# Kernel tuning notes

Hardware: AMD Instinct MI355X
Metric: run time of the kernel (lower is better)

Reference implementation:

```python
import jax, jax.numpy as jnp
import numpy as np

N_HEAD = 8


def setup_inputs() -> dict:
    key = jax.random.key(0)
    ks = jax.random.split(key, 4)
    B, L, C = 4, 1024, 512
    x = jax.random.normal(ks[0], (B, L, C), dtype=jnp.float32)
    adj = jax.random.uniform(ks[1], (B, L, L), dtype=jnp.float32)
    W_qkv = jax.random.normal(ks[2], (3 * C, C), dtype=jnp.float32) * 0.02
    W_proj = jax.random.normal(ks[3], (C, C), dtype=jnp.float32) * 0.02
    bias_scale = jnp.array([3.0, 3.0], dtype=jnp.float32)
    beta = jnp.ones((3,), dtype=jnp.float32) / 3.0
    return {"x": x, "adj": adj, "W_qkv": W_qkv, "W_proj": W_proj,
            "bias_scale": bias_scale, "beta": beta}


def _branch_attn(Q, K, V, scale, bias=None):
    # Q,K,V: [B,H,L,D]
    S = jnp.einsum('bhqd,bhkd->bhqk', Q, K) / scale
    if bias is not None:
        S = S + bias
    attn = jax.nn.softmax(S, axis=-1)
    return jnp.einsum('bhqk,bhkd->bhqd', attn, V)


def reference(x, adj, W_qkv, W_proj, bias_scale, beta):
    B, L, C = x.shape
    H = N_HEAD
    D = C // H
    scale = jnp.sqrt(jnp.float32(D))

    qkv = x @ W_qkv.T  # [B,L,3C]
    Q, K, V = jnp.split(qkv, 3, axis=-1)
    Q = Q.reshape(B, L, H, D).transpose(0, 2, 1, 3)  # [B,H,L,D]
    K = K.reshape(B, L, H, D).transpose(0, 2, 1, 3)
    V = V.reshape(B, L, H, D).transpose(0, 2, 1, 3)

    # has_cls: zero out CLS row/col in adjacency
    adj_local = adj.at[:, 0, :].set(0.0).at[:, :, 0].set(0.0)
    B_fwd = adj_local[:, None, :, :]              # [B,1,L,L]
    B_bwd = jnp.swapaxes(adj_local, -1, -2)[:, None, :, :]

    h0 = _branch_attn(Q, K, V, scale)
    h1 = _branch_attn(Q, K, V, scale, bias_scale[0] * B_fwd)
    h2 = _branch_attn(Q, K, V, scale, bias_scale[1] * B_bwd)

    b = jax.nn.softmax(beta, axis=0)
    out = b[0] * h0 + b[1] * h1 + b[2] * h2      # [B,H,L,D]
    out = out.transpose(0, 2, 1, 3).reshape(B, L, C)
    return out @ W_proj.T
```

## Files before the change

### kernel.cpp

```cpp
#include <hip/hip_runtime.h>
#include <hip/hip_bf16.h>
#include <stdint.h>

#define B_  4
#define L_  1024
#define C_  512
#define H_  8
#define D_  64
#define BH_ 32
#define M_  4096

typedef short  bf16x8 __attribute__((ext_vector_type(8)));
typedef float  f32x4  __attribute__((ext_vector_type(4)));
typedef unsigned short u16x8 __attribute__((ext_vector_type(8)));
typedef unsigned int   u32x2 __attribute__((ext_vector_type(2)));

__device__ __forceinline__ unsigned short f2bf(float f) {
    union { float f; uint32_t u; } v; v.f = f;
    uint32_t u = v.u;
    return (unsigned short)((u + 0x7fffu + ((u >> 16) & 1u)) >> 16);
}
__device__ __forceinline__ float bf2f(unsigned short s) {
    union { uint32_t u; float f; } v; v.u = ((uint32_t)s) << 16;
    return v.f;
}

__device__ __forceinline__ void gload16(const void* g, void* s) {
    __builtin_amdgcn_global_load_lds((const __attribute__((address_space(1))) void*)g,
                                     (__attribute__((address_space(3))) void*)s, 16, 0, 0);
}

__global__ void cvt_bf16(const float* __restrict__ in, unsigned short* __restrict__ out, int n4) {
    int i = blockIdx.x * blockDim.x + threadIdx.x;
    if (i < n4) {
        float4 v = ((const float4*)in)[i];
        ushort4 o;
        o.x = f2bf(v.x); o.y = f2bf(v.y); o.z = f2bf(v.z); o.w = f2bf(v.w);
        ((ushort4*)out)[i] = o;
    }
}

__global__ __launch_bounds__(256) void prep_e(const float* __restrict__ adj,
                                              const float* __restrict__ bias_scale,
                                              unsigned short* __restrict__ EI) {
    __shared__ float Tr[64][65];
    const int b = blockIdx.z, q0 = blockIdx.y * 64, k0 = blockIdx.x * 64;
    const float* adjb = adj + (size_t)b * L_ * L_;
    const int tid = threadIdx.x;
#pragma unroll
    for (int i = 0; i < 4; ++i) {
        int idx = i * 256 + tid;
        int rk = idx >> 4, c4 = (idx & 15) * 4;
        float4 v = *(const float4*)(adjb + (size_t)(k0 + rk) * L_ + q0 + c4);
        Tr[rk][c4 + 0] = v.x; Tr[rk][c4 + 1] = v.y; Tr[rk][c4 + 2] = v.z; Tr[rk][c4 + 3] = v.w;
    }
    __syncthreads();
    const float bs0 = bias_scale[0], bs1 = bias_scale[1];
    const int w = tid >> 6, l = tid & 63, g = l >> 4, c = l & 15;
#pragma unroll
    for (int qs = 0; qs < 4; ++qs) {
        int ql = qs * 16 + c, qg = q0 + ql;
        int klb = w * 16 + g * 4;
        float4 af4 = *(const float4*)(adjb + (size_t)qg * L_ + k0 + klb);
        unsigned short ef[4], eb[4];
        const float afv[4] = {af4.x, af4.y, af4.z, af4.w};
#pragma unroll
        for (int i = 0; i < 4; ++i) {
            int kg = k0 + klb + i;
            bool z = (qg == 0) || (kg == 0);
            ef[i] = f2bf(z ? 1.0f : __expf(bs0 * afv[i]));
            eb[i] = f2bf(z ? 1.0f : __expf(bs1 * Tr[klb + i][ql]));
        }
        size_t o = (((size_t)b * 64 + (blockIdx.y * 4 + qs)) * 64 + (blockIdx.x * 4 + w)) * 512 + (size_t)l * 8;
        u16x8 o8 = {ef[0], ef[1], ef[2], ef[3], eb[0], eb[1], eb[2], eb[3]};
        *(u16x8*)(EI + o) = o8;
    }
}

template <int KDIM, int NDIM, int EPI>
__global__ __launch_bounds__(256, 2) void gemm_bf16(const unsigned short* __restrict__ Amat,
                                                    const unsigned short* __restrict__ Bmat,
                                                    float* __restrict__ outp,
                                                    unsigned short* __restrict__ q_out,
                                                    unsigned short* __restrict__ k_out,
                                                    unsigned short* __restrict__ v_out) {
    __shared__ __align__(16) unsigned short As[128 * 64];
    __shared__ __align__(16) unsigned short Bs[128 * 64];
    const int tid = threadIdx.x;
    const int l = tid & 63, wid = tid >> 6;
    const int g = l >> 4, c = l & 15;
    const int wr = wid >> 1, wc = wid & 1;
    const int row0 = blockIdx.y * 128, col0 = blockIdx.x * 128;

    f32x4 acc[4][4];
#pragma unroll
    for (int mi = 0; mi < 4; ++mi)
#pragma unroll
        for (int ni = 0; ni < 4; ++ni) acc[mi][ni] = (f32x4){0.f, 0.f, 0.f, 0.f};

    for (int k0 = 0; k0 < KDIM; k0 += 64) {
        bf16x8 ra[4], rb[4];
#pragma unroll
        for (int i = 0; i < 4; ++i) {
            int q = i * 256 + tid;
            int r = q >> 3, cb = (q & 7) * 16;
            ra[i] = *(const bf16x8*)((const char*)Amat + (size_t)(row0 + r) * (KDIM * 2) + k0 * 2 + cb);
            rb[i] = *(const bf16x8*)((const char*)Bmat + (size_t)(col0 + r) * (KDIM * 2) + k0 * 2 + cb);
        }
        __syncthreads();
#pragma unroll
        for (int i = 0; i < 4; ++i) {
            int q = i * 256 + tid;
            int r = q >> 3, cb = (q & 7) * 16;
            int sw = cb ^ ((r & 7) << 4);
            *(bf16x8*)((char*)As + r * 128 + sw) = ra[i];
            *(bf16x8*)((char*)Bs + r * 128 + sw) = rb[i];
        }
        __syncthreads();
#pragma unroll
        for (int kk = 0; kk < 2; ++kk) {
            bf16x8 afr[4], bfr[4];
#pragma unroll
            for (int mi = 0; mi < 4; ++mi) {
                int r = wr * 64 + mi * 16 + c;
                afr[mi] = *(const bf16x8*)((const char*)As + r * 128 + ((kk * 64 + g * 16) ^ ((r & 7) << 4)));
            }
#pragma unroll
            for (int ni = 0; ni < 4; ++ni) {
                int r = wc * 64 + ni * 16 + c;
                bfr[ni] = *(const bf16x8*)((const char*)Bs + r * 128 + ((kk * 64 + g * 16) ^ ((r & 7) << 4)));
            }
#pragma unroll
            for (int mi = 0; mi < 4; ++mi)
#pragma unroll
                for (int ni = 0; ni < 4; ++ni)
                    acc[mi][ni] = __builtin_amdgcn_mfma_f32_16x16x32_bf16(afr[mi], bfr[ni], acc[mi][ni], 0, 0, 0);
        }
    }
#pragma unroll
    for (int mi = 0; mi < 4; ++mi) {
#pragma unroll
        for (int ni = 0; ni < 4; ++ni) {
#pragma unroll
            for (int ii = 0; ii < 4; ++ii) {
                int m = row0 + wr * 64 + mi * 16 + g * 4 + ii;
                int n = col0 + wc * 64 + ni * 16 + c;
                float val = acc[mi][ni][ii];
                if (EPI == 0) {
                    unsigned short v = f2bf(val);
                    int b = m >> 10, ll = m & 1023;
                    int which = n >> 9, cc = n & 511;
                    int hh = cc >> 6, d = cc & 63;
                    int bh = b * 8 + hh;
                    if (which == 0)      q_out[((size_t)bh * L_ + ll) * D_ + d] = v;
                    else if (which == 1) k_out[((size_t)bh * L_ + ll) * D_ + d] = v;
                    else                 v_out[((size_t)bh * D_ + d) * L_ + ll] = v;
                } else {
                    outp[(size_t)m * NDIM + n] = val;
                }
            }
        }
    }
}

__global__ __launch_bounds__(256, 2) void attn_kernel(const unsigned short* __restrict__ Qb,
                                                      const unsigned short* __restrict__ Kb,
                                                      const unsigned short* __restrict__ Vtb,
                                                      const unsigned short* __restrict__ EI,
                                                      const float* __restrict__ beta,
                                                      unsigned short* __restrict__ hb) {
    __shared__ __align__(16) char smem[2][32768];
    const int tid = threadIdx.x;
    const int w = tid >> 6, l = tid & 63;
    const int g = l >> 4, c = l & 15;
    const int bh = blockIdx.y, b = bh >> 3;
    const int q0 = blockIdx.x * 64 + w * 16;
    const int qt = blockIdx.x * 4 + w;

    const unsigned short* Qrow = Qb + ((size_t)bh * L_ + q0 + c) * D_;
    const bf16x8 qf0 = *(const bf16x8*)(Qrow + g * 8);
    const bf16x8 qf1 = *(const bf16x8*)(Qrow + 32 + g * 8);

    const unsigned short* Kbase = Kb + (size_t)bh * L_ * D_;
    const unsigned short* Vbase = Vtb + (size_t)bh * D_ * L_;
    const unsigned short* Ebase = EI + ((size_t)(b * 64 + qt) * 64) * 512;

    f32x4 O[3][4];
#pragma unroll
    for (int j = 0; j < 3; ++j)
#pragma unroll
        for (int dc = 0; dc < 4; ++dc) O[j][dc] = (f32x4){0.f, 0.f, 0.f, 0.f};
    float lsum0 = 0.f, lsum1 = 0.f, lsum2 = 0.f;

    const int srow = l >> 3, sm = l & 7;
    const int key = (c & 7) << 4;

    auto stage = [&](int t, char* base) {
#pragma unroll
        for (int n = 0; n < 2; ++n) {
            int i = 2 * w + n;
            int row = i * 8 + srow;
            int sw = (sm ^ (row & 7)) * 8;
            gload16(Kbase + (size_t)(t * 64 + row) * D_ + sw, base + i * 1024);
            gload16(Vbase + (size_t)row * L_ + t * 64 + sw, base + 8192 + i * 1024);
        }
#pragma unroll
        for (int ks = 0; ks < 4; ++ks)
            gload16(Ebase + (size_t)(t * 4 + ks) * 512 + l * 8, base + 16384 + w * 4096 + ks * 1024);
    };

    auto compute = [&](char* base) {
        char* Kl = base;
        char* Vl = base + 8192;
        char* El = base + 16384 + w * 4096;
        bf16x8 efr[4];
#pragma unroll
        for (int ks = 0; ks < 4; ++ks) efr[ks] = *(const bf16x8*)(El + ks * 1024 + l * 16);

        unsigned r[4][3][2];
#pragma unroll
        for (int st = 0; st < 4; ++st) {
            const char* kr = Kl + (st * 16 + c) * 128;
            bf16x8 ka = *(const bf16x8*)(kr + ((g * 16) ^ key));
            bf16x8 kb = *(const bf16x8*)(kr + ((64 + g * 16) ^ key));
            f32x4 s = (f32x4){0.f, 0.f, 0.f, 0.f};
            s = __builtin_amdgcn_mfma_f32_16x16x32_bf16(ka, qf0, s, 0, 0, 0);
            s = __builtin_amdgcn_mfma_f32_16x16x32_bf16(kb, qf1, s, 0, 0, 0);
            float p[3][4];
#pragma unroll
            for (int i = 0; i < 4; ++i) {
                float p0 = __expf(s[i] * 0.125f);
                float p1 = p0 * bf2f((unsigned short)efr[st][i]);
                float p2 = p0 * bf2f((unsigned short)efr[st][4 + i]);
                lsum0 += p0; lsum1 += p1; lsum2 += p2;
                p[0][i] = p0; p[1][i] = p1; p[2][i] = p2;
            }
#pragma unroll
            for (int j = 0; j < 3; ++j) {
                r[st][j][0] = __builtin_amdgcn_perm(__float_as_uint(p[j][1]), __float_as_uint(p[j][0]), 0x07060302u);
                r[st][j][1] = __builtin_amdgcn_perm(__float_as_uint(p[j][3]), __float_as_uint(p[j][2]), 0x07060302u);
            }
        }
#pragma unroll
        for (int kk = 0; kk < 2; ++kk) {
            bf16x8 af[3];
#pragma unroll
            for (int j = 0; j < 3; ++j) {
                union { unsigned u[4]; bf16x8 v; } t_;
                t_.u[0] = r[2 * kk][j][0];     t_.u[1] = r[2 * kk][j][1];
                t_.u[2] = r[2 * kk + 1][j][0]; t_.u[3] = r[2 * kk + 1][j][1];
                af[j] = t_.v;
            }
#pragma unroll
            for (int dc = 0; dc < 4; ++dc) {
                const char* vr = Vl + (dc * 16 + c) * 128;
                u32x2 vlo = *(const u32x2*)(vr + ((kk * 64 + g * 8) ^ key));
                u32x2 vhi = *(const u32x2*)(vr + ((kk * 64 + 32 + g * 8) ^ key));
                union { unsigned u[4]; bf16x8 v; } bv;
                bv.u[0] = vlo[0]; bv.u[1] = vlo[1]; bv.u[2] = vhi[0]; bv.u[3] = vhi[1];
#pragma unroll
                for (int j = 0; j < 3; ++j)
                    O[j][dc] = __builtin_amdgcn_mfma_f32_16x16x32_bf16(af[j], bv.v, O[j][dc], 0, 0, 0);
            }
        }
    };

    stage(0, smem[0]);
    __syncthreads();
#pragma unroll 1
    for (int t = 0; t < 16; t += 2) {
        stage(t + 1, smem[1]);
        compute(smem[0]);
        __syncthreads();
        if (t + 2 < 16) stage(t + 2, smem[0]);
        compute(smem[1]);
        __syncthreads();
    }

    lsum0 += __shfl_xor(lsum0, 16); lsum0 += __shfl_xor(lsum0, 32);
    lsum1 += __shfl_xor(lsum1, 16); lsum1 += __shfl_xor(lsum1, 32);
    lsum2 += __shfl_xor(lsum2, 16); lsum2 += __shfl_xor(lsum2, 32);

    float b0 = beta[0], b1 = beta[1], b2 = beta[2];
    float bm = fmaxf(b0, fmaxf(b1, b2));
    float e0 = __expf(b0 - bm), e1 = __expf(b1 - bm), e2 = __expf(b2 - bm);
    float inv = 1.0f / (e0 + e1 + e2);
    float i0 = e0 * inv / lsum0, i1 = e1 * inv / lsum1, i2 = e2 * inv / lsum2;

    float iq0[4], iq1[4], iq2[4];
#pragma unroll
    for (int ii = 0; ii < 4; ++ii) {
        iq0[ii] = __shfl(i0, g * 4 + ii);
        iq1[ii] = __shfl(i1, g * 4 + ii);
        iq2[ii] = __shfl(i2, g * 4 + ii);
    }
    const int hcol = (bh & 7) * 64;
#pragma unroll
    for (int dc = 0; dc < 4; ++dc) {
#pragma unroll
        for (int ii = 0; ii < 4; ++ii) {
            float h = iq0[ii] * O[0][dc][ii] + iq1[ii] * O[1][dc][ii] + iq2[ii] * O[2][dc][ii];
            int qrow = q0 + g * 4 + ii;
            hb[((size_t)(b << 10) + qrow) * C_ + hcol + dc * 16 + c] = f2bf(h);
        }
    }
}

extern "C" void kernel_launch(void* const* d_in, const int* in_sizes, int n_in,
                              void* d_out, int out_size, void* d_ws, size_t ws_size,
                              hipStream_t stream) {
    const float* x          = (const float*)d_in[0];
    const float* adj        = (const float*)d_in[1];
    const float* wqkv       = (const float*)d_in[2];
    const float* wproj      = (const float*)d_in[3];
    const float* bias_scale = (const float*)d_in[4];
    const float* beta       = (const float*)d_in[5];
    float* out = (float*)d_out;

    char* ws = (char*)d_ws;
    size_t off = 0;
    auto alloc = [&](size_t bytes) {
        void* p = ws + off;
        off += (bytes + 255) & ~(size_t)255;
        return p;
    };
    unsigned short* xb     = (unsigned short*)alloc((size_t)M_ * C_ * 2);
    unsigned short* wqkvb  = (unsigned short*)alloc((size_t)3 * C_ * C_ * 2);
    unsigned short* wprojb = (unsigned short*)alloc((size_t)C_ * C_ * 2);
    unsigned short* Qb     = (unsigned short*)alloc((size_t)BH_ * L_ * D_ * 2);
    unsigned short* Kb     = (unsigned short*)alloc((size_t)BH_ * L_ * D_ * 2);
    unsigned short* Vtb    = (unsigned short*)alloc((size_t)BH_ * D_ * L_ * 2);
    unsigned short* EI     = (unsigned short*)alloc((size_t)B_ * L_ * L_ * 4);
    unsigned short* hb     = (unsigned short*)alloc((size_t)M_ * C_ * 2);

    {
        int n4 = M_ * C_ / 4;
        cvt_bf16<<<(n4 + 255) / 256, 256, 0, stream>>>(x, xb, n4);
    }
    {
        int n4 = 3 * C_ * C_ / 4;
        cvt_bf16<<<(n4 + 255) / 256, 256, 0, stream>>>(wqkv, wqkvb, n4);
    }
    {
        int n4 = C_ * C_ / 4;
        cvt_bf16<<<(n4 + 255) / 256, 256, 0, stream>>>(wproj, wprojb, n4);
    }
    prep_e<<<dim3(L_ / 64, L_ / 64, B_), 256, 0, stream>>>(adj, bias_scale, EI);
    gemm_bf16<512, 1536, 0><<<dim3(1536 / 128, M_ / 128), 256, 0, stream>>>(xb, wqkvb, nullptr, Qb, Kb, Vtb);
    attn_kernel<<<dim3(L_ / 64, BH_), 256, 0, stream>>>(Qb, Kb, Vtb, EI, beta, hb);
    gemm_bf16<512, 512, 1><<<dim3(512 / 128, M_ / 128), 256, 0, stream>>>(hb, wprojb, out, nullptr, nullptr, nullptr);
}
```

Before: 82.15 us.

## Fuse conversions, shrink GEMM tiles, remap attention grid, load bias via registers

```diff
diff --git a/kernel.cpp b/kernel.cpp
--- a/kernel.cpp
+++ b/kernel.cpp
@@ -30,14 +30,23 @@
                                      (__attribute__((address_space(3))) void*)s, 16, 0, 0);
 }
 
-__global__ void cvt_bf16(const float* __restrict__ in, unsigned short* __restrict__ out, int n4) {
-    int i = blockIdx.x * blockDim.x + threadIdx.x;
-    if (i < n4) {
-        float4 v = ((const float4*)in)[i];
-        ushort4 o;
-        o.x = f2bf(v.x); o.y = f2bf(v.y); o.z = f2bf(v.z); o.w = f2bf(v.w);
-        ((ushort4*)out)[i] = o;
-    }
+#define NX4   (M_ * C_ / 4)
+#define NWQ4  (3 * C_ * C_ / 4)
+#define NWP4  (C_ * C_ / 4)
+__global__ void cvt_all(const float* __restrict__ x, const float* __restrict__ wq,
+                        const float* __restrict__ wp,
+                        unsigned short* __restrict__ xb, unsigned short* __restrict__ wqb,
+                        unsigned short* __restrict__ wpb) {
+    int i = blockIdx.x * 256 + threadIdx.x;
+    const float* src; unsigned short* dst; int o;
+    if (i < NX4) { src = x; dst = xb; o = i; }
+    else if (i < NX4 + NWQ4) { src = wq; dst = wqb; o = i - NX4; }
+    else if (i < NX4 + NWQ4 + NWP4) { src = wp; dst = wpb; o = i - NX4 - NWQ4; }
+    else return;
+    float4 v = ((const float4*)src)[o];
+    ushort4 r;
+    r.x = f2bf(v.x); r.y = f2bf(v.y); r.z = f2bf(v.z); r.w = f2bf(v.w);
+    ((ushort4*)dst)[o] = r;
 }
 
 __global__ __launch_bounds__(256) void prep_e(const float* __restrict__ adj,
@@ -77,74 +86,85 @@
     }
 }
 
-template <int KDIM, int NDIM, int EPI>
-__global__ __launch_bounds__(256, 2) void gemm_bf16(const unsigned short* __restrict__ Amat,
+template <int BM, int BN, int KDIM, int EPI, int NDIM>
+__global__ __launch_bounds__(256, 4) void gemm_bf16(const unsigned short* __restrict__ Amat,
                                                     const unsigned short* __restrict__ Bmat,
                                                     float* __restrict__ outp,
                                                     unsigned short* __restrict__ q_out,
                                                     unsigned short* __restrict__ k_out,
                                                     unsigned short* __restrict__ v_out) {
-    __shared__ __align__(16) unsigned short As[128 * 64];
-    __shared__ __align__(16) unsigned short Bs[128 * 64];
+    constexpr int NA = BM / 32, NB = BN / 32;
+    constexpr int MI = BM / 32, NI = BN / 32;
+    __shared__ __align__(16) unsigned short As[BM * 64];
+    __shared__ __align__(16) unsigned short Bs[BN * 64];
     const int tid = threadIdx.x;
     const int l = tid & 63, wid = tid >> 6;
     const int g = l >> 4, c = l & 15;
     const int wr = wid >> 1, wc = wid & 1;
-    const int row0 = blockIdx.y * 128, col0 = blockIdx.x * 128;
-
-    f32x4 acc[4][4];
-#pragma unroll
-    for (int mi = 0; mi < 4; ++mi)
-#pragma unroll
-        for (int ni = 0; ni < 4; ++ni) acc[mi][ni] = (f32x4){0.f, 0.f, 0.f, 0.f};
+    const int row0 = blockIdx.y * BM, col0 = blockIdx.x * BN;
+
+    f32x4 acc[MI][NI];
+#pragma unroll
+    for (int mi = 0; mi < MI; ++mi)
+#pragma unroll
+        for (int ni = 0; ni < NI; ++ni) acc[mi][ni] = (f32x4){0.f, 0.f, 0.f, 0.f};
 
     for (int k0 = 0; k0 < KDIM; k0 += 64) {
-        bf16x8 ra[4], rb[4];
-#pragma unroll
-        for (int i = 0; i < 4; ++i) {
+        bf16x8 ra[NA], rb[NB];
+#pragma unroll
+        for (int i = 0; i < NA; ++i) {
             int q = i * 256 + tid;
             int r = q >> 3, cb = (q & 7) * 16;
             ra[i] = *(const bf16x8*)((const char*)Amat + (size_t)(row0 + r) * (KDIM * 2) + k0 * 2 + cb);
-            rb[i] = *(const bf16x8*)((const char*)Bmat + (size_t)(col0 + r) * (KDIM * 2) + k0 * 2 + cb);
-        }
-        __syncthreads();
-#pragma unroll
-        for (int i = 0; i < 4; ++i) {
+        }
+#pragma unroll
+        for (int i = 0; i < NB; ++i) {
             int q = i * 256 + tid;
             int r = q >> 3, cb = (q & 7) * 16;
-            int sw = cb ^ ((r & 7) << 4);
-            *(bf16x8*)((char*)As + r * 128 + sw) = ra[i];
-            *(bf16x8*)((char*)Bs + r * 128 + sw) = rb[i];
+            rb[i] = *(const bf16x8*)((const char*)Bmat + (size_t)(col0 + r) * (KDIM * 2) + k0 * 2 + cb);
         }
         __syncthreads();
 #pragma unroll
+        for (int i = 0; i < NA; ++i) {
+            int q = i * 256 + tid;
+            int r = q >> 3, cb = (q & 7) * 16;
+            *(bf16x8*)((char*)As + r * 128 + (cb ^ ((r & 7) << 4))) = ra[i];
+        }
+#pragma unroll
+        for (int i = 0; i < NB; ++i) {
+            int q = i * 256 + tid;
+            int r = q >> 3, cb = (q & 7) * 16;
+            *(bf16x8*)((char*)Bs + r * 128 + (cb ^ ((r & 7) << 4))) = rb[i];
+        }
+        __syncthreads();
+#pragma unroll
         for (int kk = 0; kk < 2; ++kk) {
-            bf16x8 afr[4], bfr[4];
-#pragma unroll
-            for (int mi = 0; mi < 4; ++mi) {
-                int r = wr * 64 + mi * 16 + c;
+            bf16x8 afr[MI], bfr[NI];
+#pragma unroll
+            for (int mi = 0; mi < MI; ++mi) {
+                int r = wr * (BM / 2) + mi * 16 + c;
                 afr[mi] = *(const bf16x8*)((const char*)As + r * 128 + ((kk * 64 + g * 16) ^ ((r & 7) << 4)));
             }
 #pragma unroll
-            for (int ni = 0; ni < 4; ++ni) {
-                int r = wc * 64 + ni * 16 + c;
+            for (int ni = 0; ni < NI; ++ni) {
+                int r = wc * (BN / 2) + ni * 16 + c;
                 bfr[ni] = *(const bf16x8*)((const char*)Bs + r * 128 + ((kk * 64 + g * 16) ^ ((r & 7) << 4)));
             }
 #pragma unroll
-            for (int mi = 0; mi < 4; ++mi)
-#pragma unroll
-                for (int ni = 0; ni < 4; ++ni)
+            for (int mi = 0; mi < MI; ++mi)
+#pragma unroll
+                for (int ni = 0; ni < NI; ++ni)
                     acc[mi][ni] = __builtin_amdgcn_mfma_f32_16x16x32_bf16(afr[mi], bfr[ni], acc[mi][ni], 0, 0, 0);
         }
     }
 #pragma unroll
-    for (int mi = 0; mi < 4; ++mi) {
-#pragma unroll
-        for (int ni = 0; ni < 4; ++ni) {
+    for (int mi = 0; mi < MI; ++mi) {
+#pragma unroll
+        for (int ni = 0; ni < NI; ++ni) {
 #pragma unroll
             for (int ii = 0; ii < 4; ++ii) {
-                int m = row0 + wr * 64 + mi * 16 + g * 4 + ii;
-                int n = col0 + wc * 64 + ni * 16 + c;
+                int m = row0 + wr * (BM / 2) + mi * 16 + g * 4 + ii;
+                int n = col0 + wc * (BN / 2) + ni * 16 + c;
                 float val = acc[mi][ni][ii];
                 if (EPI == 0) {
                     unsigned short v = f2bf(val);
@@ -163,19 +183,26 @@
     }
 }
 
+struct EReg { bf16x8 e[4]; };
+
 __global__ __launch_bounds__(256, 2) void attn_kernel(const unsigned short* __restrict__ Qb,
                                                       const unsigned short* __restrict__ Kb,
                                                       const unsigned short* __restrict__ Vtb,
                                                       const unsigned short* __restrict__ EI,
                                                       const float* __restrict__ beta,
                                                       unsigned short* __restrict__ hb) {
-    __shared__ __align__(16) char smem[2][32768];
+    __shared__ __align__(16) char smem[2][16384];
     const int tid = threadIdx.x;
     const int w = tid >> 6, l = tid & 63;
     const int g = l >> 4, c = l & 15;
-    const int bh = blockIdx.y, b = bh >> 3;
-    const int q0 = blockIdx.x * 64 + w * 16;
-    const int qt = blockIdx.x * 4 + w;
+
+    const int p = blockIdx.x;
+    const int s = (p & 7) + 8 * (p >> 6);
+    const int h = (p >> 3) & 7;
+    const int b = s >> 4, qb = s & 15;
+    const int bh = b * 8 + h;
+    const int q0 = qb * 64 + w * 16;
+    const int qt = qb * 4 + w;
 
     const unsigned short* Qrow = Qb + ((size_t)bh * L_ + q0 + c) * D_;
     const bf16x8 qf0 = *(const bf16x8*)(Qrow + g * 8);
@@ -204,41 +231,38 @@
             gload16(Kbase + (size_t)(t * 64 + row) * D_ + sw, base + i * 1024);
             gload16(Vbase + (size_t)row * L_ + t * 64 + sw, base + 8192 + i * 1024);
         }
+    };
+    auto eload = [&](EReg& X, int t) {
 #pragma unroll
         for (int ks = 0; ks < 4; ++ks)
-            gload16(Ebase + (size_t)(t * 4 + ks) * 512 + l * 8, base + 16384 + w * 4096 + ks * 1024);
+            X.e[ks] = *(const bf16x8*)(Ebase + (size_t)(t * 4 + ks) * 512 + l * 8);
     };
 
-    auto compute = [&](char* base) {
-        char* Kl = base;
-        char* Vl = base + 8192;
-        char* El = base + 16384 + w * 4096;
-        bf16x8 efr[4];
-#pragma unroll
-        for (int ks = 0; ks < 4; ++ks) efr[ks] = *(const bf16x8*)(El + ks * 1024 + l * 16);
-
+    auto compute = [&](const char* base, const EReg& E) {
+        const char* Kl = base;
+        const char* Vl = base + 8192;
         unsigned r[4][3][2];
 #pragma unroll
         for (int st = 0; st < 4; ++st) {
             const char* kr = Kl + (st * 16 + c) * 128;
             bf16x8 ka = *(const bf16x8*)(kr + ((g * 16) ^ key));
             bf16x8 kb = *(const bf16x8*)(kr + ((64 + g * 16) ^ key));
-            f32x4 s = (f32x4){0.f, 0.f, 0.f, 0.f};
-            s = __builtin_amdgcn_mfma_f32_16x16x32_bf16(ka, qf0, s, 0, 0, 0);
-            s = __builtin_amdgcn_mfma_f32_16x16x32_bf16(kb, qf1, s, 0, 0, 0);
-            float p[3][4];
+            f32x4 sacc = (f32x4){0.f, 0.f, 0.f, 0.f};
+            sacc = __builtin_amdgcn_mfma_f32_16x16x32_bf16(ka, qf0, sacc, 0, 0, 0);
+            sacc = __builtin_amdgcn_mfma_f32_16x16x32_bf16(kb, qf1, sacc, 0, 0, 0);
+            float pv[3][4];
 #pragma unroll
             for (int i = 0; i < 4; ++i) {
-                float p0 = __expf(s[i] * 0.125f);
-                float p1 = p0 * bf2f((unsigned short)efr[st][i]);
-                float p2 = p0 * bf2f((unsigned short)efr[st][4 + i]);
+                float p0 = __expf(sacc[i] * 0.125f);
+                float p1 = p0 * bf2f((unsigned short)E.e[st][i]);
+                float p2 = p0 * bf2f((unsigned short)E.e[st][4 + i]);
                 lsum0 += p0; lsum1 += p1; lsum2 += p2;
-                p[0][i] = p0; p[1][i] = p1; p[2][i] = p2;
+                pv[0][i] = p0; pv[1][i] = p1; pv[2][i] = p2;
             }
 #pragma unroll
             for (int j = 0; j < 3; ++j) {
-                r[st][j][0] = __builtin_amdgcn_perm(__float_as_uint(p[j][1]), __float_as_uint(p[j][0]), 0x07060302u);
-                r[st][j][1] = __builtin_amdgcn_perm(__float_as_uint(p[j][3]), __float_as_uint(p[j][2]), 0x07060302u);
+                r[st][j][0] = __builtin_amdgcn_perm(__float_as_uint(pv[j][1]), __float_as_uint(pv[j][0]), 0x07060302u);
+                r[st][j][1] = __builtin_amdgcn_perm(__float_as_uint(pv[j][3]), __float_as_uint(pv[j][2]), 0x07060302u);
             }
         }
 #pragma unroll
@@ -265,15 +289,18 @@
         }
     };
 
+    EReg E0, E1;
     stage(0, smem[0]);
+    eload(E0, 0);
     __syncthreads();
 #pragma unroll 1
     for (int t = 0; t < 16; t += 2) {
         stage(t + 1, smem[1]);
-        compute(smem[0]);
+        eload(E1, t + 1);
+        compute(smem[0], E0);
         __syncthreads();
-        if (t + 2 < 16) stage(t + 2, smem[0]);
-        compute(smem[1]);
+        if (t + 2 < 16) { stage(t + 2, smem[0]); eload(E0, t + 2); }
+        compute(smem[1], E1);
         __syncthreads();
     }
 
@@ -299,9 +326,9 @@
     for (int dc = 0; dc < 4; ++dc) {
 #pragma unroll
         for (int ii = 0; ii < 4; ++ii) {
-            float h = iq0[ii] * O[0][dc][ii] + iq1[ii] * O[1][dc][ii] + iq2[ii] * O[2][dc][ii];
+            float hv = iq0[ii] * O[0][dc][ii] + iq1[ii] * O[1][dc][ii] + iq2[ii] * O[2][dc][ii];
             int qrow = q0 + g * 4 + ii;
-            hb[((size_t)(b << 10) + qrow) * C_ + hcol + dc * 16 + c] = f2bf(h);
+            hb[((size_t)(b << 10) + qrow) * C_ + hcol + dc * 16 + c] = f2bf(hv);
         }
     }
 }
@@ -333,20 +360,9 @@
     unsigned short* EI     = (unsigned short*)alloc((size_t)B_ * L_ * L_ * 4);
     unsigned short* hb     = (unsigned short*)alloc((size_t)M_ * C_ * 2);
 
-    {
-        int n4 = M_ * C_ / 4;
-        cvt_bf16<<<(n4 + 255) / 256, 256, 0, stream>>>(x, xb, n4);
-    }
-    {
-        int n4 = 3 * C_ * C_ / 4;
-        cvt_bf16<<<(n4 + 255) / 256, 256, 0, stream>>>(wqkv, wqkvb, n4);
-    }
-    {
-        int n4 = C_ * C_ / 4;
-        cvt_bf16<<<(n4 + 255) / 256, 256, 0, stream>>>(wproj, wprojb, n4);
-    }
+    cvt_all<<<(NX4 + NWQ4 + NWP4 + 255) / 256, 256, 0, stream>>>(x, wqkv, wproj, xb, wqkvb, wprojb);
     prep_e<<<dim3(L_ / 64, L_ / 64, B_), 256, 0, stream>>>(adj, bias_scale, EI);
-    gemm_bf16<512, 1536, 0><<<dim3(1536 / 128, M_ / 128), 256, 0, stream>>>(xb, wqkvb, nullptr, Qb, Kb, Vtb);
-    attn_kernel<<<dim3(L_ / 64, BH_), 256, 0, stream>>>(Qb, Kb, Vtb, EI, beta, hb);
-    gemm_bf16<512, 512, 1><<<dim3(512 / 128, M_ / 128), 256, 0, stream>>>(hb, wprojb, out, nullptr, nullptr, nullptr);
-}
+    gemm_bf16<64, 128, 512, 0, 0><<<dim3(1536 / 128, M_ / 64), 256, 0, stream>>>(xb, wqkvb, nullptr, Qb, Kb, Vtb);
+    attn_kernel<<<dim3(512), 256, 0, stream>>>(Qb, Kb, Vtb, EI, beta, hb);
+    gemm_bf16<64, 64, 512, 1, 512><<<dim3(512 / 64, M_ / 64), 256, 0, stream>>>(hb, wprojb, out, nullptr, nullptr, nullptr);
+}
```

Measured after the change: 71.84 us. 1.14x faster.
